# Kernel tuning notes

Hardware: AMD Instinct MI355X
Metric: run time of the kernel (lower is better)

Reference implementation:

```python
import jax, jax.numpy as jnp
import numpy as np

C = 1024
H = C // 64          # 16 heads
CH = 64              # head dim
NUM_BUCKETS = 32
MAX_DISTANCE = 64
REL_SCALE = float(np.sqrt(CH))  # (channels//num_heads)**0.5 = 8
EPS = 1e-5


def group_norm(x, gamma, beta, groups):
    # x: [B, C, T]
    B, Cc, T = x.shape
    xg = x.reshape(B, groups, -1)
    m = xg.mean(-1, keepdims=True)
    v = xg.var(-1, keepdims=True)
    xn = ((xg - m) * jax.lax.rsqrt(v + EPS)).reshape(B, Cc, T)
    return xn * gamma[None, :, None] + beta[None, :, None]


def conv1d(x, w, b, pad):
    # x: [B, Cin, T], w: [Cout, Cin, K]
    y = jax.lax.conv_general_dilated(x, w, (1,), [(pad, pad)],
                                     dimension_numbers=('NCH', 'OIH', 'NCH'))
    return y + b[None, :, None]


def rel_pos_bias(T, emb):
    # lucidrains RelativePositionBias, non-causal; emb: [num_buckets, H]
    pos = jnp.arange(T)
    n = pos[:, None] - pos[None, :]          # n = -(k - q) = q - k
    half = NUM_BUCKETS // 2                  # 16
    ret = (n < 0).astype(jnp.int32) * half
    n = jnp.abs(n)
    max_exact = half // 2                    # 8
    is_small = n < max_exact
    nf = jnp.maximum(n, 1).astype(jnp.float32)
    val_large = max_exact + (jnp.log(nf / max_exact)
                             / np.log(MAX_DISTANCE / max_exact)
                             * (half - max_exact)).astype(jnp.int32)
    val_large = jnp.minimum(val_large, half - 1)
    bucket = ret + jnp.where(is_small, n, val_large)  # [T, T]
    return emb[bucket].transpose(2, 0, 1)             # [H, T, T]


def setup_inputs() -> dict:
    key = jax.random.key(0)
    ks = jax.random.split(key, 20)
    B, T = 8, 1024
    s = 0.02
    return {
        'x': jax.random.normal(ks[0], (B, C, T), jnp.float32),
        # ResBlock in_layers
        'rb_gn1_g': jnp.ones((C,), jnp.float32),
        'rb_gn1_b': jnp.zeros((C,), jnp.float32),
        'rb_conv1_w': jax.random.normal(ks[1], (C, C, 3), jnp.float32) * s,
        'rb_conv1_b': jnp.zeros((C,), jnp.float32),
        # ResBlock out_layers (zero-init in original; randomized for testing)
        'rb_gn2_g': jnp.ones((C,), jnp.float32),
        'rb_gn2_b': jnp.zeros((C,), jnp.float32),
        'rb_conv2_w': jax.random.normal(ks[2], (C, C, 3), jnp.float32) * s,
        'rb_conv2_b': jnp.zeros((C,), jnp.float32),
        # outer GroupNorm(8, C)
        'norm_g': jnp.ones((C,), jnp.float32),
        'norm_b': jnp.zeros((C,), jnp.float32),
        # AttentionBlock
        'attn_gn_g': jnp.ones((C,), jnp.float32),
        'attn_gn_b': jnp.zeros((C,), jnp.float32),
        'qkv_w': jax.random.normal(ks[3], (3 * C, C, 1), jnp.float32) * s,
        'qkv_b': jnp.zeros((3 * C,), jnp.float32),
        'proj_w': jax.random.normal(ks[4], (C, C, 1), jnp.float32) * s,
        'proj_b': jnp.zeros((C,), jnp.float32),
        'rel_emb': jax.random.normal(ks[5], (NUM_BUCKETS, H), jnp.float32) * s,
    }


def reference(x, rb_gn1_g, rb_gn1_b, rb_conv1_w, rb_conv1_b,
              rb_gn2_g, rb_gn2_b, rb_conv2_w, rb_conv2_b,
              norm_g, norm_b, attn_gn_g, attn_gn_b,
              qkv_w, qkv_b, proj_w, proj_b, rel_emb):
    B, Cc, T = x.shape
    # ResBlock: GN32 -> SiLU -> conv3 -> GN32 -> SiLU -> (dropout=0) -> conv3, + skip
    h = jax.nn.silu(group_norm(x, rb_gn1_g, rb_gn1_b, 32))
    h = conv1d(h, rb_conv1_w, rb_conv1_b, 1)
    h = jax.nn.silu(group_norm(h, rb_gn2_g, rb_gn2_b, 32))
    h = conv1d(h, rb_conv2_w, rb_conv2_b, 1)
    h = x + h
    # outer GroupNorm(8)
    h = group_norm(h, norm_g, norm_b, 8)
    # AttentionBlock with relative position bias
    xin = h
    qkv = conv1d(group_norm(h, attn_gn_g, attn_gn_b, 32), qkv_w, qkv_b, 0)
    # channel layout after reshape(bs*H, 3*ch, T): [H, 3, ch]
    qkv = qkv.reshape(B, H, 3, CH, T)
    q, k, v = qkv[:, :, 0], qkv[:, :, 1], qkv[:, :, 2]
    scale = CH ** -0.25
    w = jnp.einsum('bhct,bhcs->bhts', q * scale, k * scale)
    bias = rel_pos_bias(T, rel_emb) * REL_SCALE       # [H, T, T]
    w = jax.nn.softmax((w + bias[None]).astype(jnp.float32), axis=-1).astype(w.dtype)
    a = jnp.einsum('bhts,bhcs->bhct', w, v).reshape(B, Cc, T)
    return xin + conv1d(a, proj_w, proj_b, 0)
```

## Files before the change

kernel.cpp:

```cpp
#include <hip/hip_runtime.h>

typedef __attribute__((ext_vector_type(4))) float f32x4;
typedef __attribute__((ext_vector_type(8))) __bf16 bf16x8;
typedef __attribute__((ext_vector_type(4))) unsigned short us4;
typedef __attribute__((ext_vector_type(8))) unsigned short us8;

#define DEVI static __device__ __forceinline__

DEVI unsigned short f2bf(float f){
  union { float f; unsigned u; } x; x.f = f;
  unsigned r = x.u + 0x7fffu + ((x.u >> 16) & 1u);
  return (unsigned short)(r >> 16);
}
DEVI float bf2f(unsigned short h){
  union { unsigned u; float f; } x; x.u = ((unsigned)h) << 16;
  return x.f;
}

typedef __attribute__((address_space(1))) unsigned int gu32;
typedef __attribute__((address_space(3))) unsigned int lu32;
DEVI void gll16(const void* g, void* l){
  __builtin_amdgcn_global_load_lds((gu32*)g, (lu32*)l, 16, 0, 0);
}

DEVI f32x4 mfma16(bf16x8 a, bf16x8 b, f32x4 c){
  return __builtin_amdgcn_mfma_f32_16x16x32_bf16(a, b, c, 0, 0, 0);
}

DEVI float wredsum(float v){
  #pragma unroll
  for (int m = 1; m < 64; m <<= 1) v += __shfl_xor(v, m);
  return v;
}

__global__ __launch_bounds__(256) void conv_w_prep(const float* __restrict__ w,
                                                   unsigned short* __restrict__ wp){
  int idx = blockIdx.x * 256 + threadIdx.x;
  const float* p = w + (size_t)idx * 3;
  wp[idx]           = f2bf(p[0]);
  wp[1048576 + idx] = f2bf(p[1]);
  wp[2097152 + idx] = f2bf(p[2]);
}

__global__ __launch_bounds__(256) void cast_f2b(const float* __restrict__ in,
                                                unsigned short* __restrict__ out, int n4){
  int idx = blockIdx.x * 256 + threadIdx.x;
  if (idx < n4){
    f32x4 v = *(const f32x4*)&in[(size_t)idx * 4];
    us4 o;
    #pragma unroll
    for (int j = 0; j < 4; j++) o[j] = f2bf(v[j]);
    *(us4*)&out[(size_t)idx * 4] = o;
  }
}

__global__ __launch_bounds__(256) void btab_k(const float* __restrict__ emb,
                                              float* __restrict__ btab){
  int idx = blockIdx.x * 256 + threadIdx.x;
  if (idx >= 2047 * 16) return;
  int d = idx >> 4, h = idx & 15;
  int n0 = d - 1023;
  int ret = (n0 < 0) ? 16 : 0;
  int n = (n0 < 0) ? -n0 : n0;
  int bucket;
  if (n < 8) bucket = ret + n;
  else {
    float ratio = logf((float)n * 0.125f) / 2.0794415416798357f;
    int vl = 8 + (int)(ratio * 8.0f);
    bucket = ret + (vl < 15 ? vl : 15);
  }
  btab[h * 2048 + d] = emb[bucket * 16 + h] * 11.541560327111707f;
}

__global__ __launch_bounds__(256) void zero_pads(unsigned short* __restrict__ h1p,
                                                 unsigned short* __restrict__ g2p){
  int idx = blockIdx.x * 256 + threadIdx.x;
  int b = idx >> 11, rr = (idx >> 10) & 1, c = idx & 1023;
  size_t off = ((size_t)b * 1026 + (rr ? 1025 : 0)) * 1024 + c;
  h1p[off] = 0; g2p[off] = 0;
}

__global__ __launch_bounds__(256) void gn_stats_cast(const float* __restrict__ in,
                                                     float2* __restrict__ st,
                                                     unsigned short* __restrict__ xb){
  const int g = blockIdx.x; const int tid = threadIdx.x;
  const float* p = in + (size_t)g * 32768;
  unsigned short* q = xb + (size_t)g * 32768;
  float s = 0.f, s2 = 0.f;
  for (int i = tid * 4; i < 32768; i += 1024){
    f32x4 v = *(const f32x4*)&p[i];
    us4 o;
    #pragma unroll
    for (int j = 0; j < 4; j++){ s += v[j]; s2 += v[j] * v[j]; o[j] = f2bf(v[j]); }
    *(us4*)&q[i] = o;
  }
  s = wredsum(s); s2 = wredsum(s2);
  __shared__ float rs[4], rs2[4];
  if ((tid & 63) == 0){ rs[tid >> 6] = s; rs2[tid >> 6] = s2; }
  __syncthreads();
  if (tid == 0){
    float S = rs[0] + rs[1] + rs[2] + rs[3];
    float S2 = rs2[0] + rs2[1] + rs2[2] + rs2[3];
    float m = S * (1.f / 32768.f);
    float var = S2 * (1.f / 32768.f) - m * m;
    st[g] = make_float2(m, rsqrtf(var + 1e-5f));
  }
}

template<int SILU, int INBF16, int OUTPAD, int FROMPART>
__global__ __launch_bounds__(256) void gn_apply_tr(
    const void* __restrict__ inp, const float2* __restrict__ st,
    const float* __restrict__ gma, const float* __restrict__ bta,
    unsigned short* __restrict__ out)
{
  const int gid = blockIdx.x;
  const int tc = gid & 15, g = (gid >> 4) & 31, b = gid >> 9;
  const int tid = threadIdx.x;
  const int t0 = tc * 64;
  __shared__ __align__(16) unsigned short tr[64 * 40];
  float2 s;
  if (FROMPART){
    int g8 = g >> 2, k = g & 3;
    float S = 0.f, S2 = 0.f;
    #pragma unroll
    for (int j = 0; j < 4; j++){
      float2 v = st[(size_t)(b * 8 + g8) * 16 + k * 4 + j];
      S += v.x; S2 += v.y;
    }
    float m = S * (1.f / 32768.f);
    float var = S2 * (1.f / 32768.f) - m * m;
    s = make_float2(m, rsqrtf(var + 1e-5f));
  } else {
    s = st[b * 32 + g];
  }
  int c = tid >> 3, t8 = (tid & 7) * 8;
  int ch = g * 32 + c;
  float sc = gma[ch] * s.y;
  float sh = bta[ch] - s.x * sc;
  float vv[8];
  if (INBF16){
    const unsigned short* p = (const unsigned short*)inp + ((size_t)b * 1024 + ch) * 1024 + t0 + t8;
    us8 v = *(const us8*)p;
    #pragma unroll
    for (int j = 0; j < 8; j++) vv[j] = bf2f(v[j]);
  } else {
    const float* p = (const float*)inp + ((size_t)b * 1024 + ch) * 1024 + t0 + t8;
    f32x4 v0 = *(const f32x4*)p; f32x4 v1 = *(const f32x4*)(p + 4);
    #pragma unroll
    for (int j = 0; j < 4; j++){ vv[j] = v0[j]; vv[4 + j] = v1[j]; }
  }
  #pragma unroll
  for (int j = 0; j < 8; j++){
    float v = vv[j] * sc + sh;
    if (SILU) v = v / (1.f + __expf(-v));
    tr[(t8 + j) * 40 + c] = f2bf(v);
  }
  __syncthreads();
  int t = tid >> 2, c8 = (tid & 3) * 8;
  us8 d = *(const us8*)&tr[t * 40 + c8];
  size_t row = OUTPAD ? ((size_t)b * 1026 + 1 + t0 + t) : ((size_t)b * 1024 + t0 + t);
  *(us8*)&out[row * 1024 + g * 32 + c8] = d;
}

template<int SILU>
__global__ __launch_bounds__(256) void gn2_apply(const unsigned short* __restrict__ c1,
    const float2* __restrict__ part2, const float* __restrict__ gma, const float* __restrict__ bta,
    unsigned short* __restrict__ outp)
{
  const int tid = threadIdx.x;
  const int ck = blockIdx.x & 31, b = blockIdx.x >> 5;
  const int g = tid >> 3;
  float S = 0.f, S2 = 0.f;
  #pragma unroll
  for (int tt = 0; tt < 8; tt++){
    float2 v = part2[(size_t)(b * 8 + tt) * 32 + g];
    S += v.x; S2 += v.y;
  }
  float mm = S * (1.f / 32768.f);
  float var = S2 * (1.f / 32768.f) - mm * mm;
  float2 s = make_float2(mm, rsqrtf(var + 1e-5f));
  float sc[4], sh[4];
  #pragma unroll
  for (int j = 0; j < 4; j++){ int ch = tid * 4 + j; sc[j] = gma[ch] * s.y; sh[j] = bta[ch] - s.x * sc[j]; }
  const unsigned short* p = c1 + ((size_t)b * 1024 + ck * 32) * 1024 + tid * 4;
  unsigned short* q = outp + ((size_t)b * 1026 + 1 + ck * 32) * 1024 + tid * 4;
  for (int r = 0; r < 32; r++){
    us4 v = *(const us4*)&p[(size_t)r * 1024];
    us4 o;
    #pragma unroll
    for (int j = 0; j < 4; j++){
      float f = bf2f(v[j]) * sc[j] + sh[j];
      if (SILU) f = f / (1.f + __expf(-f));
      o[j] = f2bf(f);
    }
    *(us4*)&q[(size_t)r * 1024] = o;
  }
}

__global__ __launch_bounds__(256) void gn8_apply(const unsigned short* __restrict__ r,
    const float2* __restrict__ part8, const float* __restrict__ gma, const float* __restrict__ bta,
    unsigned short* __restrict__ xin, float2* __restrict__ part32){
  const int gid = blockIdx.x; const int tid = threadIdx.x;
  const int sub = gid & 15, g = (gid >> 4) & 7, b = gid >> 7;
  float S = 0.f, S2 = 0.f;
  #pragma unroll
  for (int tt = 0; tt < 8; tt++){
    float2 v = part8[(size_t)(b * 8 + tt) * 8 + g];
    S += v.x; S2 += v.y;
  }
  float mm = S * (1.f / 131072.f);
  float var = S2 * (1.f / 131072.f) - mm * mm;
  float2 s = make_float2(mm, rsqrtf(var + 1e-5f));
  const unsigned short* pr = r + ((size_t)(b * 8 + g)) * 131072 + sub * 8192;
  unsigned short* px = xin + ((size_t)(b * 8 + g)) * 131072 + sub * 8192;
  float ps = 0.f, ps2 = 0.f;
  for (int i = tid * 8; i < 8192; i += 2048){
    int c = g * 128 + sub * 8 + (i >> 10);
    float sc = gma[c] * s.y, sh = bta[c] - s.x * sc;
    us8 v = *(const us8*)&pr[i];
    us8 o;
    #pragma unroll
    for (int j = 0; j < 8; j++){
      float f = bf2f(v[j]) * sc + sh;
      ps += f; ps2 += f * f;
      o[j] = f2bf(f);
    }
    *(us8*)&px[i] = o;
  }
  ps = wredsum(ps); ps2 = wredsum(ps2);
  __shared__ float rs[4], rs2[4];
  if ((tid & 63) == 0){ rs[tid >> 6] = ps; rs2[tid >> 6] = ps2; }
  __syncthreads();
  if (tid == 0)
    part32[(size_t)(b * 8 + g) * 16 + sub] =
      make_float2(rs[0] + rs[1] + rs[2] + rs[3], rs2[0] + rs2[1] + rs2[2] + rs2[3]);
}

template<int KK, int EPI, int GPART>
__global__ __launch_bounds__(256, 2) void gemm_k(
    const unsigned short* __restrict__ inT,
    const unsigned short* __restrict__ W,
    const float* __restrict__ bias,
    void* __restrict__ outp,
    void* __restrict__ resp,
    float2* __restrict__ part,
    int OC, int NT)
{
  __shared__ __align__(16) unsigned short Alds[2][128 * 64];
  __shared__ __align__(16) unsigned short Blds[2][128 * 64];
  __shared__ float sred[16];
  const int tid = threadIdx.x;
  const int lane = tid & 63;
  const int w = tid >> 6;
  const int wn = w >> 1, wo = w & 1;
  const int nt = blockIdx.x % NT;
  const int ot = blockIdx.x / NT;
  const int b = nt >> 3;
  const int t0 = (nt & 7) * 128;
  const int ob = ot * 128;
  const int rowbase = (KK == 3) ? (b * 1026 + t0) : (b * 1024 + t0);
  const int NTI = KK * 16;

  f32x4 acc[4][4];
  #pragma unroll
  for (int m = 0; m < 4; m++)
    #pragma unroll
    for (int n = 0; n < 4; n++) acc[m][n] = 0.f;

  const int lrow = lane >> 3;
  const int lblk = lane & 7;

  auto stage = [&](int kt, int bufsel){
    int kk = kt >> 4;
    int i0 = (kt & 15) * 64;
    const unsigned short* Ab = inT + (size_t)(rowbase + kk) * 1024;
    const unsigned short* Bb = W + ((size_t)kk * OC + ob) * 1024;
    #pragma unroll
    for (int j = 0; j < 4; ++j){
      int chunk = w * 4 + j;
      int row = chunk * 8 + lrow;
      int gcol = (lblk ^ (row & 7)) * 8;
      gll16(Ab + (size_t)row * 1024 + i0 + gcol, &Alds[bufsel][chunk * 512]);
      gll16(Bb + (size_t)row * 1024 + i0 + gcol, &Blds[bufsel][chunk * 512]);
    }
  };

  stage(0, 0);
  stage(1, 1);
  asm volatile("s_waitcnt vmcnt(8)" ::: "memory");
  __builtin_amdgcn_sched_barrier(0);
  __builtin_amdgcn_s_barrier();
  __builtin_amdgcn_sched_barrier(0);

  #pragma unroll 2
  for (int kt = 0; kt < NTI; ++kt){
    const int cur = kt & 1;
    const unsigned short* Ab = &Alds[cur][0];
    const unsigned short* Bb = &Blds[cur][0];
    bf16x8 af[2][4], bfv[2][4];
    #pragma unroll
    for (int m = 0; m < 4; m++){
      int row = wn * 64 + m * 16 + (lane & 15);
      #pragma unroll
      for (int k2 = 0; k2 < 2; k2++){
        int blk = ((lane >> 4) + k2 * 4) ^ (row & 7);
        af[k2][m] = *(const bf16x8*)&Ab[row * 64 + blk * 8];
      }
    }
    #pragma unroll
    for (int n = 0; n < 4; n++){
      int row = wo * 64 + n * 16 + (lane & 15);
      #pragma unroll
      for (int k2 = 0; k2 < 2; k2++){
        int blk = ((lane >> 4) + k2 * 4) ^ (row & 7);
        bfv[k2][n] = *(const bf16x8*)&Bb[row * 64 + blk * 8];
      }
    }
    asm volatile("s_waitcnt lgkmcnt(0)" ::: "memory");
    __builtin_amdgcn_sched_barrier(0);
    __builtin_amdgcn_s_barrier();
    __builtin_amdgcn_sched_barrier(0);
    if (kt + 2 < NTI) stage(kt + 2, cur);
    __builtin_amdgcn_sched_barrier(0);
    __builtin_amdgcn_s_setprio(1);
    #pragma unroll
    for (int k2 = 0; k2 < 2; k2++)
      #pragma unroll
      for (int m = 0; m < 4; m++)
        #pragma unroll
        for (int n = 0; n < 4; n++)
          acc[m][n] = mfma16(af[k2][m], bfv[k2][n], acc[m][n]);
    __builtin_amdgcn_s_setprio(0);
    __builtin_amdgcn_sched_barrier(0);
    if (kt + 2 < NTI){ asm volatile("s_waitcnt vmcnt(8)" ::: "memory"); }
    else             { asm volatile("s_waitcnt vmcnt(0)" ::: "memory"); }
    __builtin_amdgcn_sched_barrier(0);
    __builtin_amdgcn_s_barrier();
    __builtin_amdgcn_sched_barrier(0);
  }

  if (EPI == 0){
    unsigned short* out = (unsigned short*)outp;
    float ps[2] = {0.f, 0.f}, ps2[2] = {0.f, 0.f};
    #pragma unroll
    for (int m = 0; m < 4; m++){
      int tl = t0 + wn * 64 + m * 16 + ((lane >> 4) * 4);
      #pragma unroll
      for (int n = 0; n < 4; n++){
        int o = ob + wo * 64 + n * 16 + (lane & 15);
        float bz = bias[o];
        size_t base = ((size_t)b * 1024 + tl) * OC + o;
        #pragma unroll
        for (int r = 0; r < 4; r++){
          float v = acc[m][n][r] + bz;
          if (GPART == 2){ ps[n >> 1] += v; ps2[n >> 1] += v * v; }
          out[base + (size_t)r * OC] = f2bf(v);
        }
      }
    }
    if (GPART == 2){
      #pragma unroll
      for (int j = 0; j < 2; j++){ ps[j] = wredsum(ps[j]); ps2[j] = wredsum(ps2[j]); }
      if (lane == 0){
        sred[w * 4 + 0] = ps[0]; sred[w * 4 + 1] = ps2[0];
        sred[w * 4 + 2] = ps[1]; sred[w * 4 + 3] = ps2[1];
      }
      __syncthreads();
      if (tid < 4){
        int g = tid, woo = g >> 1, jj = g & 1;
        float S  = sred[woo * 4 + jj * 2 + 0] + sred[(woo + 2) * 4 + jj * 2 + 0];
        float S2 = sred[woo * 4 + jj * 2 + 1] + sred[(woo + 2) * 4 + jj * 2 + 1];
        part[(size_t)(b * 8 + (nt & 7)) * 32 + ot * 4 + g] = make_float2(S, S2);
      }
    }
  } else if (EPI == 3){
    unsigned short* qkT = (unsigned short*)outp;
    unsigned short* vT  = (unsigned short*)resp;
    #pragma unroll
    for (int m = 0; m < 4; m++){
      int tl = t0 + wn * 64 + m * 16 + ((lane >> 4) * 4);
      #pragma unroll
      for (int n = 0; n < 4; n++){
        int o0 = ob + wo * 64 + n * 16;
        int h = o0 / 192;
        int rem0 = o0 - h * 192;
        int o = o0 + (lane & 15);
        float bz = bias[o];
        if (rem0 < 128){
          size_t base = ((size_t)b * 1024 + tl) * 2048 + h * 128 + rem0 + (lane & 15);
          #pragma unroll
          for (int r = 0; r < 4; r++)
            qkT[base + (size_t)r * 2048] = f2bf(acc[m][n][r] + bz);
        } else {
          int c = rem0 - 128 + (lane & 15);
          size_t base = (((size_t)(b * 16 + h)) * 64 + c) * 1024 + tl;
          us4 o4;
          #pragma unroll
          for (int r = 0; r < 4; r++) o4[r] = f2bf(acc[m][n][r] + bz);
          *(us4*)&vT[base] = o4;
        }
      }
    }
  } else if (EPI == 4){
    unsigned short* out = (unsigned short*)outp;
    const unsigned short* xr = (const unsigned short*)resp;
    float ps = 0.f, ps2 = 0.f;
    #pragma unroll
    for (int m = 0; m < 4; m++){
      int tl = t0 + wn * 64 + m * 16 + ((lane >> 4) * 4);
      #pragma unroll
      for (int n = 0; n < 4; n++){
        int o = ob + wo * 64 + n * 16 + (lane & 15);
        float bz = bias[o];
        size_t base = ((size_t)b * 1024 + o) * 1024 + tl;
        us4 xv = *(const us4*)&xr[base];
        us4 ov;
        #pragma unroll
        for (int r = 0; r < 4; r++){
          float v = bf2f(xv[r]) + acc[m][n][r] + bz;
          if (GPART == 8){ ps += v; ps2 += v * v; }
          ov[r] = f2bf(v);
        }
        *(us4*)&out[base] = ov;
      }
    }
    if (GPART == 8){
      ps = wredsum(ps); ps2 = wredsum(ps2);
      if (lane == 0){ sred[w * 2] = ps; sred[w * 2 + 1] = ps2; }
      __syncthreads();
      if (tid == 0){
        float S = sred[0] + sred[2] + sred[4] + sred[6];
        float S2 = sred[1] + sred[3] + sred[5] + sred[7];
        part[(size_t)(b * 8 + (nt & 7)) * 8 + ot] = make_float2(S, S2);
      }
    }
  } else {
    float* out = (float*)outp;
    #pragma unroll
    for (int m = 0; m < 4; m++){
      int tl = t0 + wn * 64 + m * 16 + ((lane >> 4) * 4);
      #pragma unroll
      for (int n = 0; n < 4; n++){
        int o = ob + wo * 64 + n * 16 + (lane & 15);
        float bz = bias[o];
        size_t base = ((size_t)b * 1024 + o) * 1024 + tl;
        const unsigned short* xr = (const unsigned short*)resp;
        us4 xv = *(const us4*)&xr[base];
        f32x4 v;
        v[0] = bf2f(xv[0]); v[1] = bf2f(xv[1]); v[2] = bf2f(xv[2]); v[3] = bf2f(xv[3]);
        #pragma unroll
        for (int r = 0; r < 4; r++) v[r] += acc[m][n][r] + bz;
        *(f32x4*)&out[base] = v;
      }
    }
  }
}

__global__ __launch_bounds__(256, 3) void attn_k7(
    const unsigned short* __restrict__ qkT,
    const unsigned short* __restrict__ vT,
    const float* __restrict__ btab,
    unsigned short* __restrict__ aT)
{
  __shared__ __align__(16) unsigned short Kb[2][64 * 64];
  __shared__ __align__(16) unsigned short Vb[2][64 * 64];
  __shared__ __align__(16) unsigned short Pb[4][32 * 64];
  __shared__ __align__(16) float blds[1152];
  const int tid = threadIdx.x, lane = tid & 63, w = tid >> 6;
  const int d0 = blockIdx.x;
  const int xcd = d0 & 7, slot = d0 >> 3;
  const int bh = xcd * 16 + (slot >> 3);
  const int qt = slot & 7;
  const int h = bh & 15, b = bh >> 4;
  const int q0b = qt * 128;
  const int q0 = q0b + w * 32;
  const unsigned short* qk = qkT + (size_t)b * 1024 * 2048 + h * 128;
  const unsigned short* vh = vT + ((size_t)(b * 16 + h)) * 64 * 1024;
  const int lc = lane & 15, lg = lane >> 4;

  const float bneg = btab[h * 2048 + 0];
  const float bpos = btab[h * 2048 + 2046];

  for (int i = tid; i < 1151; i += 256)
    blds[i] = btab[h * 2048 + q0b + i];

  bf16x8 qf[2][2];
  #pragma unroll
  for (int m = 0; m < 2; m++){
    const unsigned short* qrow = qk + (size_t)(q0 + m * 16 + lc) * 2048;
    #pragma unroll
    for (int k2 = 0; k2 < 2; k2++)
      qf[m][k2] = *(const bf16x8*)&qrow[k2 * 32 + lg * 8];
  }
  float l_run[2];
  f32x4 oacc[2][4];
  l_run[0] = l_run[1] = 0.f;
  #pragma unroll
  for (int m = 0; m < 2; m++)
    #pragma unroll
    for (int cb = 0; cb < 4; cb++) oacc[m][cb] = 0.f;

  const int lr = lane >> 3, lb = lane & 7;
  const float qs = 0.18033688011112042f;

  #pragma unroll
  for (int j = 0; j < 2; j++){
    int chunk = w * 2 + j;
    int row = chunk * 8 + lr;
    int gcol = (lb ^ (row & 7)) * 8;
    gll16(qk + 64 + (size_t)row * 2048 + gcol, &Kb[0][chunk * 512]);
    gll16(vh + (size_t)row * 1024 + gcol, &Vb[0][chunk * 512]);
  }
  __syncthreads();

  for (int t = 0; t < 16; ++t){
    const int cur = t & 1;
    const int st0 = t * 64;
    if (t < 15){
      int nst = st0 + 64;
      #pragma unroll
      for (int j = 0; j < 2; j++){
        int chunk = w * 2 + j;
        int row = chunk * 8 + lr;
        int gcol = (lb ^ (row & 7)) * 8;
        gll16(qk + 64 + (size_t)(nst + row) * 2048 + gcol, &Kb[cur ^ 1][chunk * 512]);
        gll16(vh + (size_t)row * 1024 + nst + gcol, &Vb[cur ^ 1][chunk * 512]);
      }
    }
    f32x4 sfr[2][4];
    #pragma unroll
    for (int m = 0; m < 2; m++)
      #pragma unroll
      for (int sub = 0; sub < 4; sub++) sfr[m][sub] = 0.f;
    __builtin_amdgcn_s_setprio(1);
    #pragma unroll
    for (int sub = 0; sub < 4; sub++){
      int row = sub * 16 + lc;
      #pragma unroll
      for (int k2 = 0; k2 < 2; k2++){
        int blk = (lg + k2 * 4) ^ (row & 7);
        bf16x8 bk = *(const bf16x8*)&Kb[cur][row * 64 + blk * 8];
        sfr[0][sub] = mfma16(bk, qf[0][k2], sfr[0][sub]);
        sfr[1][sub] = mfma16(bk, qf[1][k2], sfr[1][sub]);
      }
    }
    __builtin_amdgcn_s_setprio(0);
    const bool unineg = (st0 >= q0 + 81);
    const bool unipos = (st0 + 113 <= q0);
    const bool uni = unineg || unipos;
    const float bc = unineg ? bneg : bpos;
    if (uni){
      #pragma unroll
      for (int m = 0; m < 2; m++){
        float ssum = 0.f;
        #pragma unroll
        for (int sub = 0; sub < 4; sub++)
          #pragma unroll
          for (int r = 0; r < 4; r++){
            float e = exp2f(fmaf(sfr[m][sub][r], qs, bc));
            sfr[m][sub][r] = e;
            ssum += e;
          }
        ssum += __shfl_xor(ssum, 16);
        ssum += __shfl_xor(ssum, 32);
        l_run[m] += ssum;
      }
    } else {
      #pragma unroll
      for (int m = 0; m < 2; m++){
        const float* bp = &blds[(w * 32 + m * 16 + lc) + 960 - st0];
        float ssum = 0.f;
        #pragma unroll
        for (int sub = 0; sub < 4; sub++){
          int off = 63 - sub * 16 - lg * 4;
          #pragma unroll
          for (int r = 0; r < 4; r++){
            float e = exp2f(fmaf(sfr[m][sub][r], qs, bp[off - r]));
            sfr[m][sub][r] = e;
            ssum += e;
          }
        }
        ssum += __shfl_xor(ssum, 16);
        ssum += __shfl_xor(ssum, 32);
        l_run[m] += ssum;
      }
    }
    unsigned short* P = &Pb[w][0];
    #pragma unroll
    for (int m = 0; m < 2; m++){
      int qrow = m * 16 + lc;
      int rsw = (qrow & 7) << 3;
      #pragma unroll
      for (int sub = 0; sub < 4; sub++){
        int col = sub * 16 + lg * 4;
        unsigned w0, w1;
        asm("v_cvt_pk_bf16_f32 %0, %1, %2" : "=v"(w0) : "v"(sfr[m][sub][0]), "v"(sfr[m][sub][1]));
        asm("v_cvt_pk_bf16_f32 %0, %1, %2" : "=v"(w1) : "v"(sfr[m][sub][2]), "v"(sfr[m][sub][3]));
        uint2 pk; pk.x = w0; pk.y = w1;
        *(uint2*)&P[qrow * 64 + (col ^ rsw)] = pk;
      }
    }
    __builtin_amdgcn_s_setprio(1);
    #pragma unroll
    for (int k2 = 0; k2 < 2; k2++){
      bf16x8 pa[2];
      #pragma unroll
      for (int m = 0; m < 2; m++){
        int rowp = m * 16 + lc;
        int blkp = (lg + k2 * 4) ^ (rowp & 7);
        pa[m] = *(const bf16x8*)&P[rowp * 64 + blkp * 8];
      }
      #pragma unroll
      for (int cb = 0; cb < 4; cb++){
        int ch = cb * 16 + lc;
        int blkv = (lg + k2 * 4) ^ (ch & 7);
        bf16x8 bv = *(const bf16x8*)&Vb[cur][ch * 64 + blkv * 8];
        oacc[0][cb] = mfma16(pa[0], bv, oacc[0][cb]);
        oacc[1][cb] = mfma16(pa[1], bv, oacc[1][cb]);
      }
    }
    __builtin_amdgcn_s_setprio(0);
    __syncthreads();
  }
  #pragma unroll
  for (int m = 0; m < 2; m++)
    #pragma unroll
    for (int r = 0; r < 4; r++){
      float li = 1.0f / __shfl(l_run[m], lg * 4 + r);
      int tq = q0 + m * 16 + lg * 4 + r;
      #pragma unroll
      for (int cb = 0; cb < 4; cb++){
        int ch = h * 64 + cb * 16 + lc;
        aT[((size_t)b * 1024 + tq) * 1024 + ch] = f2bf(oacc[m][cb][r] * li);
      }
    }
}

extern "C" void kernel_launch(void* const* d_in, const int* in_sizes, int n_in,
                              void* d_out, int out_size, void* d_ws, size_t ws_size,
                              hipStream_t stream)
{
  const float* x       = (const float*)d_in[0];
  const float* gn1_g   = (const float*)d_in[1];
  const float* gn1_b   = (const float*)d_in[2];
  const float* conv1_w = (const float*)d_in[3];
  const float* conv1_b = (const float*)d_in[4];
  const float* gn2_g   = (const float*)d_in[5];
  const float* gn2_b   = (const float*)d_in[6];
  const float* conv2_w = (const float*)d_in[7];
  const float* conv2_b = (const float*)d_in[8];
  const float* norm_g  = (const float*)d_in[9];
  const float* norm_b  = (const float*)d_in[10];
  const float* agn_g   = (const float*)d_in[11];
  const float* agn_b   = (const float*)d_in[12];
  const float* qkv_w   = (const float*)d_in[13];
  const float* qkv_b   = (const float*)d_in[14];
  const float* proj_w  = (const float*)d_in[15];
  const float* proj_b  = (const float*)d_in[16];
  const float* rel_emb = (const float*)d_in[17];

  if (ws_size < 139526144u) return;

  char* ws = (char*)d_ws;
  unsigned short* w1p   = (unsigned short*)(ws + 0);
  unsigned short* w2p   = (unsigned short*)(ws + 6291456);
  unsigned short* wqkv  = (unsigned short*)(ws + 12582912);
  unsigned short* wproj = (unsigned short*)(ws + 18874368);
  float* btab           = (float*)(ws + 20971520);
  float2* stats1        = (float2*)(ws + 21102592);
  float2* part2n        = (float2*)(ws + 21110784);
  float2* part8n        = (float2*)(ws + 21127168);
  float2* part32        = (float2*)(ws + 21131264);
  unsigned short* h1p   = (unsigned short*)(ws + 22020096);
  unsigned short* c1    = (unsigned short*)(ws + 38830080);
  unsigned short* g2p   = (unsigned short*)(ws + 55607296);
  unsigned short* qkT   = h1p;
  unsigned short* vT    = (unsigned short*)(ws + 55574528);
  unsigned short* xb    = (unsigned short*)(ws + 72417280);
  unsigned short* attn_in = (unsigned short*)(ws + 72417280);
  unsigned short* xin   = (unsigned short*)(ws + 105971712);
  unsigned short* aT    = (unsigned short*)(ws + 122748928);

  conv_w_prep<<<4096, 256, 0, stream>>>(conv1_w, w1p);
  conv_w_prep<<<4096, 256, 0, stream>>>(conv2_w, w2p);
  cast_f2b<<<3072, 256, 0, stream>>>(qkv_w, wqkv, 3072 * 1024 / 4);
  cast_f2b<<<1024, 256, 0, stream>>>(proj_w, wproj, 1024 * 1024 / 4);
  btab_k<<<128, 256, 0, stream>>>(rel_emb, btab);
  zero_pads<<<64, 256, 0, stream>>>(h1p, g2p);

  gn_stats_cast<<<256, 256, 0, stream>>>(x, stats1, xb);
  gn_apply_tr<1, 1, 1, 0><<<4096, 256, 0, stream>>>(xb, stats1, gn1_g, gn1_b, h1p);

  gemm_k<3, 0, 2><<<512, 256, 0, stream>>>(h1p, w1p, conv1_b, c1, nullptr, part2n, 1024, 64);
  gn2_apply<1><<<256, 256, 0, stream>>>(c1, part2n, gn2_g, gn2_b, g2p);

  gemm_k<3, 4, 8><<<512, 256, 0, stream>>>(g2p, w2p, conv2_b, xb, xb, part8n, 1024, 64);
  gn8_apply<<<1024, 256, 0, stream>>>(xb, part8n, norm_g, norm_b, xin, part32);

  gn_apply_tr<0, 1, 0, 1><<<4096, 256, 0, stream>>>(xin, part32, agn_g, agn_b, attn_in);

  gemm_k<1, 3, 0><<<1536, 256, 0, stream>>>(attn_in, wqkv, qkv_b, qkT, vT, nullptr, 3072, 64);

  attn_k7<<<1024, 256, 0, stream>>>(qkT, vT, btab, aT);

  gemm_k<1, 2, 0><<<512, 256, 0, stream>>>(aT, wproj, proj_b, d_out, xin, nullptr, 1024, 64);
}
```

Baseline: 347.2 us.

## Merge prep kernels, remap GEMM blocks per XCD, compute softmax sums via MFMA

The six small prep launches are merged into three: conv weight prep, weight casts, and a kernel that zeroes pads and builds the bias table. This cuts launch overhead. GEMM block indices are permuted so that consecutive tiles land on the same XCD, which should improve L2 reuse. In attention, the per-row softmax denominator now comes from an extra MFMA against a ones vector instead of shuffle reductions, and the bias LDS window is shrunk to a compact 288-entry table. The extra MFMAs add matrix work, and the denominator now sums the bf16-rounded probabilities rather than fp32 values.

```diff
diff --git a/kernel.cpp b/kernel.cpp
--- a/kernel.cpp
+++ b/kernel.cpp
@@ -33,51 +33,61 @@
   return v;
 }
 
-__global__ __launch_bounds__(256) void conv_w_prep(const float* __restrict__ w,
-                                                   unsigned short* __restrict__ wp){
+__global__ __launch_bounds__(256) void conv_w_prep2(const float* __restrict__ w1,
+                                                    const float* __restrict__ w2,
+                                                    unsigned short* __restrict__ wp1,
+                                                    unsigned short* __restrict__ wp2){
   int idx = blockIdx.x * 256 + threadIdx.x;
-  const float* p = w + (size_t)idx * 3;
-  wp[idx]           = f2bf(p[0]);
-  wp[1048576 + idx] = f2bf(p[1]);
-  wp[2097152 + idx] = f2bf(p[2]);
-}
-
-__global__ __launch_bounds__(256) void cast_f2b(const float* __restrict__ in,
-                                                unsigned short* __restrict__ out, int n4){
+  int sel = idx >> 20;
+  int lo  = idx & 1048575;
+  const float* p = (sel ? w2 : w1) + (size_t)lo * 3;
+  unsigned short* wp = sel ? wp2 : wp1;
+  wp[lo]           = f2bf(p[0]);
+  wp[1048576 + lo] = f2bf(p[1]);
+  wp[2097152 + lo] = f2bf(p[2]);
+}
+
+__global__ __launch_bounds__(256) void cast_f2b2(const float* __restrict__ qw,
+                                                 const float* __restrict__ pw,
+                                                 unsigned short* __restrict__ qo,
+                                                 unsigned short* __restrict__ po){
   int idx = blockIdx.x * 256 + threadIdx.x;
-  if (idx < n4){
-    f32x4 v = *(const f32x4*)&in[(size_t)idx * 4];
-    us4 o;
-    #pragma unroll
-    for (int j = 0; j < 4; j++) o[j] = f2bf(v[j]);
-    *(us4*)&out[(size_t)idx * 4] = o;
-  }
-}
-
-__global__ __launch_bounds__(256) void btab_k(const float* __restrict__ emb,
-                                              float* __restrict__ btab){
-  int idx = blockIdx.x * 256 + threadIdx.x;
-  if (idx >= 2047 * 16) return;
-  int d = idx >> 4, h = idx & 15;
-  int n0 = d - 1023;
-  int ret = (n0 < 0) ? 16 : 0;
-  int n = (n0 < 0) ? -n0 : n0;
-  int bucket;
-  if (n < 8) bucket = ret + n;
-  else {
-    float ratio = logf((float)n * 0.125f) / 2.0794415416798357f;
-    int vl = 8 + (int)(ratio * 8.0f);
-    bucket = ret + (vl < 15 ? vl : 15);
-  }
-  btab[h * 2048 + d] = emb[bucket * 16 + h] * 11.541560327111707f;
-}
-
-__global__ __launch_bounds__(256) void zero_pads(unsigned short* __restrict__ h1p,
-                                                 unsigned short* __restrict__ g2p){
-  int idx = blockIdx.x * 256 + threadIdx.x;
-  int b = idx >> 11, rr = (idx >> 10) & 1, c = idx & 1023;
-  size_t off = ((size_t)b * 1026 + (rr ? 1025 : 0)) * 1024 + c;
-  h1p[off] = 0; g2p[off] = 0;
+  const float* src; unsigned short* dst; int lo;
+  if (idx < 786432){ src = qw; dst = qo; lo = idx; }
+  else             { src = pw; dst = po; lo = idx - 786432; }
+  f32x4 v = *(const f32x4*)&src[(size_t)lo * 4];
+  us4 o;
+  #pragma unroll
+  for (int j = 0; j < 4; j++) o[j] = f2bf(v[j]);
+  *(us4*)&dst[(size_t)lo * 4] = o;
+}
+
+__global__ __launch_bounds__(256) void misc_prep(unsigned short* __restrict__ h1p,
+                                                 unsigned short* __restrict__ g2p,
+                                                 const float* __restrict__ emb,
+                                                 float* __restrict__ btab){
+  int bid = blockIdx.x;
+  if (bid < 64){
+    int idx = bid * 256 + threadIdx.x;
+    int b = idx >> 11, rr = (idx >> 10) & 1, c = idx & 1023;
+    size_t off = ((size_t)b * 1026 + (rr ? 1025 : 0)) * 1024 + c;
+    h1p[off] = 0; g2p[off] = 0;
+  } else {
+    int idx = (bid - 64) * 256 + threadIdx.x;
+    if (idx >= 2047 * 16) return;
+    int d = idx >> 4, h = idx & 15;
+    int n0 = d - 1023;
+    int ret = (n0 < 0) ? 16 : 0;
+    int n = (n0 < 0) ? -n0 : n0;
+    int bucket;
+    if (n < 8) bucket = ret + n;
+    else {
+      float ratio = logf((float)n * 0.125f) / 2.0794415416798357f;
+      int vl = 8 + (int)(ratio * 8.0f);
+      bucket = ret + (vl < 15 ? vl : 15);
+    }
+    btab[h * 2048 + d] = emb[bucket * 16 + h] * 11.541560327111707f;
+  }
 }
 
 __global__ __launch_bounds__(256) void gn_stats_cast(const float* __restrict__ in,
@@ -253,8 +263,10 @@
   const int lane = tid & 63;
   const int w = tid >> 6;
   const int wn = w >> 1, wo = w & 1;
-  const int nt = blockIdx.x % NT;
-  const int ot = blockIdx.x / NT;
+  const int nb8 = gridDim.x >> 3;
+  const int wgid = (blockIdx.x & 7) * nb8 + (blockIdx.x >> 3);
+  const int nt = wgid % NT;
+  const int ot = wgid / NT;
   const int b = nt >> 3;
   const int t0 = (nt & 7) * 128;
   const int ob = ot * 128;
@@ -456,7 +468,7 @@
   }
 }
 
-__global__ __launch_bounds__(256, 3) void attn_k7(
+__global__ __launch_bounds__(256, 3) void attn_k9(
     const unsigned short* __restrict__ qkT,
     const unsigned short* __restrict__ vT,
     const float* __restrict__ btab,
@@ -465,7 +477,7 @@
   __shared__ __align__(16) unsigned short Kb[2][64 * 64];
   __shared__ __align__(16) unsigned short Vb[2][64 * 64];
   __shared__ __align__(16) unsigned short Pb[4][32 * 64];
-  __shared__ __align__(16) float blds[1152];
+  __shared__ __align__(16) float cblds[288];
   const int tid = threadIdx.x, lane = tid & 63, w = tid >> 6;
   const int d0 = blockIdx.x;
   const int xcd = d0 & 7, slot = d0 >> 3;
@@ -481,8 +493,7 @@
   const float bneg = btab[h * 2048 + 0];
   const float bpos = btab[h * 2048 + 2046];
 
-  for (int i = tid; i < 1151; i += 256)
-    blds[i] = btab[h * 2048 + q0b + i];
+  if (tid < 288) cblds[tid] = btab[h * 2048 + 879 + tid];
 
   bf16x8 qf[2][2];
   #pragma unroll
@@ -492,13 +503,20 @@
     for (int k2 = 0; k2 < 2; k2++)
       qf[m][k2] = *(const bf16x8*)&qrow[k2 * 32 + lg * 8];
   }
-  float l_run[2];
-  f32x4 oacc[2][4];
-  l_run[0] = l_run[1] = 0.f;
-  #pragma unroll
-  for (int m = 0; m < 2; m++)
+  bf16x8 onesf;
+  {
+    us8 u;
+    #pragma unroll
+    for (int j = 0; j < 8; j++) u[j] = 0x3F80;
+    onesf = *(bf16x8*)&u;
+  }
+  f32x4 oacc[2][4], lacc[2];
+  #pragma unroll
+  for (int m = 0; m < 2; m++){
     #pragma unroll
     for (int cb = 0; cb < 4; cb++) oacc[m][cb] = 0.f;
+    lacc[m] = 0.f;
+  }
 
   const int lr = lane >> 3, lb = lane & 7;
   const float qs = 0.18033688011112042f;
@@ -547,42 +565,24 @@
     __builtin_amdgcn_s_setprio(0);
     const bool unineg = (st0 >= q0 + 81);
     const bool unipos = (st0 + 113 <= q0);
-    const bool uni = unineg || unipos;
-    const float bc = unineg ? bneg : bpos;
-    if (uni){
-      #pragma unroll
-      for (int m = 0; m < 2; m++){
-        float ssum = 0.f;
+    if (unineg || unipos){
+      const float bc = unineg ? bneg : bpos;
+      #pragma unroll
+      for (int m = 0; m < 2; m++)
         #pragma unroll
         for (int sub = 0; sub < 4; sub++)
           #pragma unroll
-          for (int r = 0; r < 4; r++){
-            float e = exp2f(fmaf(sfr[m][sub][r], qs, bc));
-            sfr[m][sub][r] = e;
-            ssum += e;
-          }
-        ssum += __shfl_xor(ssum, 16);
-        ssum += __shfl_xor(ssum, 32);
-        l_run[m] += ssum;
-      }
+          for (int r = 0; r < 4; r++)
+            sfr[m][sub][r] = exp2f(fmaf(sfr[m][sub][r], qs, bc));
     } else {
       #pragma unroll
       for (int m = 0; m < 2; m++){
-        const float* bp = &blds[(w * 32 + m * 16 + lc) + 960 - st0];
-        float ssum = 0.f;
+        const float* bp = &cblds[(q0 + m * 16 + lc) - st0 + 144 - lg * 4];
         #pragma unroll
-        for (int sub = 0; sub < 4; sub++){
-          int off = 63 - sub * 16 - lg * 4;
+        for (int sub = 0; sub < 4; sub++)
           #pragma unroll
-          for (int r = 0; r < 4; r++){
-            float e = exp2f(fmaf(sfr[m][sub][r], qs, bp[off - r]));
-            sfr[m][sub][r] = e;
-            ssum += e;
-          }
-        }
-        ssum += __shfl_xor(ssum, 16);
-        ssum += __shfl_xor(ssum, 32);
-        l_run[m] += ssum;
+          for (int r = 0; r < 4; r++)
+            sfr[m][sub][r] = exp2f(fmaf(sfr[m][sub][r], qs, bp[-(sub * 16) - r]));
       }
     }
     unsigned short* P = &Pb[w][0];
@@ -618,6 +618,8 @@
         oacc[0][cb] = mfma16(pa[0], bv, oacc[0][cb]);
         oacc[1][cb] = mfma16(pa[1], bv, oacc[1][cb]);
       }
+      lacc[0] = mfma16(pa[0], onesf, lacc[0]);
+      lacc[1] = mfma16(pa[1], onesf, lacc[1]);
     }
     __builtin_amdgcn_s_setprio(0);
     __syncthreads();
@@ -626,7 +628,7 @@
   for (int m = 0; m < 2; m++)
     #pragma unroll
     for (int r = 0; r < 4; r++){
-      float li = 1.0f / __shfl(l_run[m], lg * 4 + r);
+      float li = 1.0f / lacc[m][r];
       int tq = q0 + m * 16 + lg * 4 + r;
       #pragma unroll
       for (int cb = 0; cb < 4; cb++){
@@ -681,12 +683,9 @@
   unsigned short* xin   = (unsigned short*)(ws + 105971712);
   unsigned short* aT    = (unsigned short*)(ws + 122748928);
 
-  conv_w_prep<<<4096, 256, 0, stream>>>(conv1_w, w1p);
-  conv_w_prep<<<4096, 256, 0, stream>>>(conv2_w, w2p);
-  cast_f2b<<<3072, 256, 0, stream>>>(qkv_w, wqkv, 3072 * 1024 / 4);
-  cast_f2b<<<1024, 256, 0, stream>>>(proj_w, wproj, 1024 * 1024 / 4);
-  btab_k<<<128, 256, 0, stream>>>(rel_emb, btab);
-  zero_pads<<<64, 256, 0, stream>>>(h1p, g2p);
+  conv_w_prep2<<<8192, 256, 0, stream>>>(conv1_w, conv2_w, w1p, w2p);
+  cast_f2b2<<<4096, 256, 0, stream>>>(qkv_w, proj_w, wqkv, wproj);
+  misc_prep<<<192, 256, 0, stream>>>(h1p, g2p, rel_emb, btab);
 
   gn_stats_cast<<<256, 256, 0, stream>>>(x, stats1, xb);
   gn_apply_tr<1, 1, 1, 0><<<4096, 256, 0, stream>>>(xb, stats1, gn1_g, gn1_b, h1p);
@@ -701,7 +700,7 @@
 
   gemm_k<1, 3, 0><<<1536, 256, 0, stream>>>(attn_in, wqkv, qkv_b, qkT, vT, nullptr, 3072, 64);
 
-  attn_k7<<<1024, 256, 0, stream>>>(qkT, vT, btab, aT);
+  attn_k9<<<1024, 256, 0, stream>>>(qkT, vT, btab, aT);
 
   gemm_k<1, 2, 0><<<512, 256, 0, stream>>>(aT, wproj, proj_b, d_out, xin, nullptr, 1024, 64);
 }
```

Result: slower. 372.7 us (+7.3%).
